# Kernel tuning notes

Hardware: AMD Instinct MI355X
Metric: run time of the kernel (lower is better)

## Reference

```python
import jax, jax.numpy as jnp
import numpy as np

N_NODES = 128
B = 2048
N = B * N_NODES          # 262144 total nodes
E_PER = 512
E = B * E_PER            # 1048576 edges
H = 64                   # hidden_dim == embedding_dim
EPS = 1e-5


def _layernorm(x, g, b):
    m = x.mean(-1, keepdims=True)
    v = ((x - m) ** 2).mean(-1, keepdims=True)
    return (x - m) * jax.lax.rsqrt(v + EPS) * g + b


def setup_inputs() -> dict:
    key = jax.random.key(0)
    ks = jax.random.split(key, 16)
    node_feature = jax.random.randint(ks[0], (N,), 0, N_NODES, dtype=jnp.int32)
    # edges stay within each graph's node block
    offs = (jnp.arange(E, dtype=jnp.int32) // E_PER) * N_NODES
    src = offs + jax.random.randint(ks[1], (E,), 0, N_NODES, dtype=jnp.int32)
    dst = offs + jax.random.randint(ks[2], (E,), 0, N_NODES, dtype=jnp.int32)
    edge_index = jnp.stack([src, dst], axis=1)          # [E, 2]
    batch_ptr = jnp.arange(B + 1, dtype=jnp.int32) * N_NODES
    s = 0.1
    f32 = jnp.float32
    return {
        'node_feature': node_feature,
        'edge_index': edge_index,
        'batch_ptr': batch_ptr,
        'emb': jax.random.normal(ks[3], (N_NODES, H), f32),
        'gcn_w': jax.random.normal(ks[4], (H, H), f32) * s,
        'gcn_b': jnp.zeros((H,), f32),
        'lin1_w': jax.random.normal(ks[5], (H, H), f32) * s,
        'lin1_b': jnp.zeros((H,), f32),
        'lin2_w': jax.random.normal(ks[6], (H, H), f32) * s,
        'lin2_b': jnp.zeros((H,), f32),
        'ln_g': jnp.ones((H,), f32),
        'ln_b': jnp.zeros((H,), f32),
        'ex_w1': jax.random.normal(ks[7], (H, H), f32) * s,
        'ex_b1': jnp.zeros((H,), f32),
        'ex_ln_g': jnp.ones((H,), f32),
        'ex_ln_b': jnp.zeros((H,), f32),
        'ex_w2': jax.random.normal(ks[8], (H, 1), f32) * s,
        'ex_b2': jnp.zeros((1,), f32),
    }


def _forward(node_feature, edge_index, batch_ptr, emb, gcn_w, gcn_b,
             lin1_w, lin1_b, lin2_w, lin2_b, ln_g, ln_b,
             ex_w1, ex_b1, ex_ln_g, ex_ln_b, ex_w2, ex_b2):
    x = emb[node_feature]                                # [N, H] embedding lookup
    # --- GCNConv (PyG gcn_norm: self-loops + symmetric normalization) ---
    loops = jnp.arange(N, dtype=edge_index.dtype)
    src = jnp.concatenate([edge_index[:, 0], loops])
    dst = jnp.concatenate([edge_index[:, 1], loops])
    deg = jax.ops.segment_sum(jnp.ones_like(dst, dtype=x.dtype), dst, N)
    dinv = jnp.where(deg > 0, jax.lax.rsqrt(deg), 0.0)
    norm = dinv[src] * dinv[dst]                         # [E+N]
    h = x @ gcn_w                                        # linear (no bias)
    h = jax.ops.segment_sum(norm[:, None] * h[src], dst, N) + gcn_b
    # --- Linear -> ReLU -> Linear, residual, LayerNorm ---
    h = jnp.maximum(h @ lin1_w + lin1_b, 0.0) @ lin2_w + lin2_b
    ef = _layernorm(h + x, ln_g, ln_b)                   # [N, H]
    # --- cumsum-based group mean over batch_ptr segments ---
    cs = jnp.concatenate([jnp.zeros((1, H), ef.dtype), jnp.cumsum(ef, axis=0)], 0)
    size = (batch_ptr[1:] - batch_ptr[:-1]).astype(ef.dtype)
    means = (cs[batch_ptr[1:]] - cs[batch_ptr[:-1]]) / size[:, None]   # [B, H]
    # --- exit MLP: Linear -> LayerNorm -> ReLU -> Linear ---
    exit_action = jnp.maximum(_layernorm(means @ ex_w1 + ex_b1, ex_ln_g, ex_ln_b), 0.0) @ ex_w2 + ex_b2  # [B, 1]
    # --- pairwise edge logits + triu/tril gather (directed) ---
    efb = ef.reshape(B, N_NODES, H)
    scores = jnp.einsum('bnf,bmf->bnm', efb, efb) / jnp.sqrt(jnp.asarray(H, ef.dtype))
    iu0, iu1 = np.triu_indices(N_NODES, 1)
    il0, il1 = np.tril_indices(N_NODES, -1)
    i0 = jnp.asarray(np.concatenate([iu0, il0]))
    i1 = jnp.asarray(np.concatenate([iu1, il1]))
    edge_actions = scores[:, i0, i1]                     # [B, n^2 - n]
    return jnp.concatenate([edge_actions, exit_action], axis=-1)


def reference(node_feature, edge_index, batch_ptr, emb, gcn_w, gcn_b,
              lin1_w, lin1_b, lin2_w, lin2_b, ln_g, ln_b,
              ex_w1, ex_b1, ex_ln_g, ex_ln_b, ex_w2, ex_b2):
    return _forward(node_feature, edge_index, batch_ptr, emb, gcn_w, gcn_b,
                    lin1_w, lin1_b, lin2_w, lin2_b, ln_g, ln_b,
                    ex_w1, ex_b1, ex_ln_g, ex_ln_b, ex_w2, ex_b2)
```

## Files before the change

### kernel.cpp

```cpp
#include <hip/hip_runtime.h>

typedef __bf16 bf16_t;
typedef __bf16 bf16x8 __attribute__((ext_vector_type(8)));
typedef float  f32x4  __attribute__((ext_vector_type(4)));
typedef f32x4  f32x4u __attribute__((aligned(4)));

#define LDR 72

__device__ __forceinline__ float bflo(unsigned u){ return __uint_as_float(u << 16); }
__device__ __forceinline__ float bfhi(unsigned u){ return __uint_as_float(u & 0xffff0000u); }

#define WS_MAP_OFF 24576

__global__ void prep_kernel(const float* __restrict__ emb,
                            const float* __restrict__ gcn_w,
                            const float* __restrict__ lin1_w,
                            const float* __restrict__ lin2_w,
                            bf16_t* __restrict__ ws)
{
    int t = blockIdx.x * 256 + threadIdx.x;
    bf16_t* emb_bf = ws;
    bf16_t* hw_bf  = ws + 8192;
    bf16_t* w1T    = ws + 16384;
    bf16_t* w2T    = ws + 20480;

    emb_bf[t] = (bf16_t)emb[t];
    int i = t >> 6, j = t & 63;
    float s = 0.f;
    #pragma unroll 8
    for (int k = 0; k < 64; ++k) s += emb[i*64 + k] * gcn_w[k*64 + j];
    hw_bf[t] = (bf16_t)s;
    if (t < 4096){
        int jj = t >> 6, kk = t & 63;
        w1T[t] = (bf16_t)lin1_w[kk*64 + jj];
        w2T[t] = (bf16_t)lin2_w[kk*64 + jj];
    }

    if (blockIdx.x == 0){
        __shared__ bf16_t pA[16*32];
        __shared__ bf16_t pB[16*32];
        int tid = threadIdx.x;
        for (int c = tid; c < 512; c += 256){
            int r = c >> 5, k = c & 31;
            pA[c] = (bf16_t)((k == 0) ? (float)r : ((k == 1) ? 1.f : 0.f));
            pB[c] = (bf16_t)((k == 0) ? 1.f : ((k == 1) ? (float)(128*r) : 0.f));
        }
        __syncthreads();
        if (tid < 64){
            int l15 = tid & 15, lg = tid >> 4;
            bf16x8 a  = *reinterpret_cast<const bf16x8*>(&pA[l15*32 + lg*8]);
            bf16x8 bb = *reinterpret_cast<const bf16x8*>(&pB[l15*32 + lg*8]);
            f32x4 acc = (f32x4){0.f,0.f,0.f,0.f};
            acc = __builtin_amdgcn_mfma_f32_16x16x32_bf16(a, bb, acc, 0, 0, 0);
            int* map = (int*)(ws + WS_MAP_OFF);
            int mi[4], mj[4];
            #pragma unroll
            for (int r = 0; r < 4; ++r){
                int iv = (int)(acc[r] + 0.5f);
                mi[r] = iv & 127; mj[r] = iv >> 7;
                map[tid*4 + r] = mi[r] | (mj[r] << 8);
            }
            bool ok = (mi[0]==mi[1] && mi[1]==mi[2] && mi[2]==mi[3] &&
                       mj[1]==mj[0]+1 && mj[2]==mj[0]+2 && mj[3]==mj[0]+3 &&
                       (mj[0] & 3) == 0);
            unsigned long long all = __ballot(ok);
            if (tid == 0) map[256] = (all == ~0ull) ? 1 : 0;
        }
    }
}

__global__ __launch_bounds__(256, 4) void fused_kernel(
    const int*   __restrict__ node_feature,
    const int*   __restrict__ edge_index,
    const float* __restrict__ gcn_b,
    const float* __restrict__ lin1_b,
    const float* __restrict__ lin2_b,
    const float* __restrict__ ln_g,
    const float* __restrict__ ln_b,
    const float* __restrict__ ex_w1,
    const float* __restrict__ ex_b1,
    const float* __restrict__ ex_ln_g,
    const float* __restrict__ ex_ln_b,
    const float* __restrict__ ex_w2,
    const float* __restrict__ ex_b2,
    const bf16_t* __restrict__ ws,
    float* __restrict__ out)
{
    __shared__ __align__(16) bf16_t bufB[128*LDR];
    __shared__ __align__(16) bf16_t bufC[128*LDR];
    __shared__ __align__(8)  unsigned char pool[2176];
    __shared__ unsigned char s_nf8[128];

    unsigned char* s_adj   = pool;
    int*           s_start = (int*)(pool + 512);
    int*           s_cur   = (int*)(pool + 1040);
    float*         s_dinv  = (float*)(pool + 1552);
    float*         s_pm    = (float*)pool;
    float*         s_means = (float*)(pool + 1024);

    const int tid  = threadIdx.x;
    const int b    = blockIdx.x;
    const int wid  = tid >> 6;
    const int lane = tid & 63;
    const int l15  = lane & 15;
    const int lg   = lane >> 4;
    const long obase = (long)b * 16257;

    const bf16_t* emb_bf = ws;
    const bf16_t* hw_bf  = ws + 8192;
    const bf16_t* w1T    = ws + 16384;
    const bf16_t* w2T    = ws + 20480;

    int mi[4], mj[4], vflag;
    {
        const int* map = (const int*)(ws + WS_MAP_OFF);
        #pragma unroll
        for (int r = 0; r < 4; ++r){
            int m = map[lane*4 + r];
            mi[r] = m & 255; mj[r] = m >> 8;
        }
        vflag = map[256];
    }

    const int2* ei = reinterpret_cast<const int2*>(edge_index) + b*512;
    int2 e0 = ei[tid];
    int2 e1 = ei[tid + 256];

    if (tid < 128) s_nf8[tid] = (unsigned char)node_feature[b*128 + tid];
    else           s_cur[tid - 128] = 0;
    __syncthreads();

    atomicAdd(&s_cur[e0.y & 127], 1);
    atomicAdd(&s_cur[e1.y & 127], 1);
    #pragma unroll
    for (int c = tid; c < 1024; c += 256){
        int row = c >> 3, ch = c & 7;
        uint4 vh = reinterpret_cast<const uint4*>(hw_bf + (int)s_nf8[row]*64)[ch];
        reinterpret_cast<uint4*>(&bufB[row*LDR])[ch] = vh;
    }
    __syncthreads();

    if (tid < 64){
        int a0 = s_cur[2*tid], a1 = s_cur[2*tid+1];
        s_dinv[2*tid]   = rsqrtf((float)(a0 + 1));
        s_dinv[2*tid+1] = rsqrtf((float)(a1 + 1));
        int s = a0 + a1;
        #pragma unroll
        for (int d = 1; d < 64; d <<= 1){
            int v = __shfl_up(s, d);
            if (lane >= d) s += v;
        }
        int excl = s - (a0 + a1);
        s_start[2*tid]   = excl;
        s_start[2*tid+1] = excl + a0;
        if (tid == 63) s_start[128] = 512;
        s_cur[2*tid]   = excl;
        s_cur[2*tid+1] = excl + a0;
    }
    __syncthreads();

    {
        int pos0 = atomicAdd(&s_cur[e0.y & 127], 1);
        s_adj[pos0] = (unsigned char)(e0.x & 127);
        int pos1 = atomicAdd(&s_cur[e1.y & 127], 1);
        s_adj[pos1] = (unsigned char)(e1.x & 127);
    }
    __syncthreads();

    {
        const int n  = tid >> 1;
        const int f0 = (tid & 1) << 5;
        float inner[32];
        #pragma unroll
        for (int f = 0; f < 32; ++f) inner[f] = 0.f;
        const float dn = s_dinv[n];
        {
            const uint4* hv = reinterpret_cast<const uint4*>(&bufB[n*LDR + f0]);
            #pragma unroll
            for (int q = 0; q < 4; ++q){
                uint4 v = hv[q];
                inner[q*8+0] += dn * bflo(v.x); inner[q*8+1] += dn * bfhi(v.x);
                inner[q*8+2] += dn * bflo(v.y); inner[q*8+3] += dn * bfhi(v.y);
                inner[q*8+4] += dn * bflo(v.z); inner[q*8+5] += dn * bfhi(v.z);
                inner[q*8+6] += dn * bflo(v.w); inner[q*8+7] += dn * bfhi(v.w);
            }
        }
        const int st = s_start[n], cn = s_start[n+1] - st;
        for (int k = 0; k < cn; ++k){
            int src = s_adj[st + k];
            float w = s_dinv[src];
            const uint4* hv = reinterpret_cast<const uint4*>(&bufB[src*LDR + f0]);
            #pragma unroll
            for (int q = 0; q < 4; ++q){
                uint4 v = hv[q];
                inner[q*8+0] += w * bflo(v.x); inner[q*8+1] += w * bfhi(v.x);
                inner[q*8+2] += w * bflo(v.y); inner[q*8+3] += w * bfhi(v.y);
                inner[q*8+4] += w * bflo(v.z); inner[q*8+5] += w * bfhi(v.z);
                inner[q*8+6] += w * bflo(v.w); inner[q*8+7] += w * bfhi(v.w);
            }
        }
        const float* gb = gcn_b + f0;
        #pragma unroll
        for (int f = 0; f < 32; ++f)
            bufC[n*LDR + f0 + f] = (bf16_t)(dn * inner[f] + gb[f]);
    }
    __syncthreads();

    {
        bf16x8 af[2][2];
        #pragma unroll
        for (int fm = 0; fm < 2; ++fm)
            #pragma unroll
            for (int kk = 0; kk < 2; ++kk)
                af[fm][kk] = *reinterpret_cast<const bf16x8*>(
                    &bufC[(wid*32 + fm*16 + l15)*LDR + kk*32 + lg*8]);
        f32x4 acc[2][4];
        #pragma unroll
        for (int fm = 0; fm < 2; ++fm)
            #pragma unroll
            for (int fn = 0; fn < 4; ++fn)
                acc[fm][fn] = (f32x4){0.f,0.f,0.f,0.f};
        #pragma unroll
        for (int fn = 0; fn < 4; ++fn)
            #pragma unroll
            for (int kk = 0; kk < 2; ++kk){
                bf16x8 bfr = *reinterpret_cast<const bf16x8*>(
                    &w1T[(fn*16 + l15)*64 + kk*32 + lg*8]);
                #pragma unroll
                for (int fm = 0; fm < 2; ++fm)
                    acc[fm][fn] = __builtin_amdgcn_mfma_f32_16x16x32_bf16(
                        af[fm][kk], bfr, acc[fm][fn], 0, 0, 0);
            }
        #pragma unroll
        for (int fm = 0; fm < 2; ++fm)
            #pragma unroll
            for (int fn = 0; fn < 4; ++fn)
                #pragma unroll
                for (int r = 0; r < 4; ++r){
                    int row = wid*32 + fm*16 + mi[r];
                    int col = fn*16 + mj[r];
                    bufB[row*LDR + col] = (bf16_t)fmaxf(acc[fm][fn][r] + lin1_b[col], 0.f);
                }
    }
    __syncthreads();

    {
        bf16x8 af[2][2];
        #pragma unroll
        for (int fm = 0; fm < 2; ++fm)
            #pragma unroll
            for (int kk = 0; kk < 2; ++kk)
                af[fm][kk] = *reinterpret_cast<const bf16x8*>(
                    &bufB[(wid*32 + fm*16 + l15)*LDR + kk*32 + lg*8]);
        f32x4 acc[2][4];
        #pragma unroll
        for (int fm = 0; fm < 2; ++fm)
            #pragma unroll
            for (int fn = 0; fn < 4; ++fn)
                acc[fm][fn] = (f32x4){0.f,0.f,0.f,0.f};
        #pragma unroll
        for (int fn = 0; fn < 4; ++fn)
            #pragma unroll
            for (int kk = 0; kk < 2; ++kk){
                bf16x8 bfr = *reinterpret_cast<const bf16x8*>(
                    &w2T[(fn*16 + l15)*64 + kk*32 + lg*8]);
                #pragma unroll
                for (int fm = 0; fm < 2; ++fm)
                    acc[fm][fn] = __builtin_amdgcn_mfma_f32_16x16x32_bf16(
                        af[fm][kk], bfr, acc[fm][fn], 0, 0, 0);
            }
        #pragma unroll
        for (int fm = 0; fm < 2; ++fm)
            #pragma unroll
            for (int fn = 0; fn < 4; ++fn)
                #pragma unroll
                for (int r = 0; r < 4; ++r){
                    int row = wid*32 + fm*16 + mi[r];
                    int col = fn*16 + mj[r];
                    bufC[row*LDR + col] = (bf16_t)(acc[fm][fn][r] + lin2_b[col]);
                }
    }
    __syncthreads();

    {
        const int n  = tid >> 1;
        const int f0 = (tid & 1) << 5;
        const bf16x8* xp = reinterpret_cast<const bf16x8*>(&emb_bf[(int)s_nf8[n]*64 + f0]);
        const bf16x8* rp = reinterpret_cast<const bf16x8*>(&bufC[n*LDR + f0]);
        float vv[32];
        float p1 = 0.f, p2 = 0.f;
        #pragma unroll
        for (int q = 0; q < 4; ++q){
            bf16x8 v8 = rp[q];
            bf16x8 x8 = xp[q];
            #pragma unroll
            for (int e = 0; e < 8; ++e){
                float f = (float)v8[e] + (float)x8[e];
                vv[q*8+e] = f; p1 += f; p2 += f*f;
            }
        }
        p1 += __shfl_xor(p1, 1);
        p2 += __shfl_xor(p2, 1);
        float mean = p1 * 0.015625f;
        float var  = p2 * 0.015625f - mean*mean;
        float rstd = rsqrtf(var + 1e-5f);
        const float* lg_ = ln_g + f0;
        const float* lb_ = ln_b + f0;
        #pragma unroll
        for (int j = 0; j < 32; ++j)
            bufC[n*LDR + f0 + j] = (bf16_t)((vv[j] - mean) * rstd * lg_[j] + lb_[j]);
    }
    __syncthreads();

    {
        int col = tid & 63, q = tid >> 6;
        float s = 0.f;
        #pragma unroll 8
        for (int r = q*32; r < q*32 + 32; ++r)
            s += (float)bufC[r*LDR + col];
        s_pm[q*64 + col] = s;
    }
    __syncthreads();
    if (tid < 64)
        s_means[tid] = (s_pm[tid] + s_pm[64+tid] + s_pm[128+tid] + s_pm[192+tid]) * 0.0078125f;
    __syncthreads();

    if (tid < 64){
        float a = ex_b1[lane];
        #pragma unroll 8
        for (int k = 0; k < 64; ++k)
            a += s_means[k] * ex_w1[k*64 + lane];
        float p1 = a, p2 = a*a;
        #pragma unroll
        for (int m = 1; m < 64; m <<= 1){ p1 += __shfl_xor(p1, m); p2 += __shfl_xor(p2, m); }
        float mean = p1 * 0.015625f;
        float var  = p2 * 0.015625f - mean*mean;
        float u = (a - mean) * rsqrtf(var + 1e-5f) * ex_ln_g[lane] + ex_ln_b[lane];
        u = fmaxf(u, 0.f);
        float prod = u * ex_w2[lane];
        #pragma unroll
        for (int m = 1; m < 64; m <<= 1) prod += __shfl_xor(prod, m);
        if (lane == 0) out[obase + 16256] = prod + ex_b2[0];
    }

    {
        bf16x8 af[2][2];
        #pragma unroll
        for (int fm = 0; fm < 2; ++fm)
            #pragma unroll
            for (int kk = 0; kk < 2; ++kk)
                af[fm][kk] = *reinterpret_cast<const bf16x8*>(
                    &bufC[(wid*32 + fm*16 + l15)*LDR + kk*32 + lg*8]);
        f32x4 acc[2][8];
        #pragma unroll
        for (int fm = 0; fm < 2; ++fm)
            #pragma unroll
            for (int fn = 0; fn < 8; ++fn)
                acc[fm][fn] = (f32x4){0.f,0.f,0.f,0.f};
        #pragma unroll
        for (int fn = 0; fn < 8; ++fn)
            #pragma unroll
            for (int kk = 0; kk < 2; ++kk){
                bf16x8 bfr = *reinterpret_cast<const bf16x8*>(
                    &bufC[(fn*16 + l15)*LDR + kk*32 + lg*8]);
                #pragma unroll
                for (int fm = 0; fm < 2; ++fm)
                    acc[fm][fn] = __builtin_amdgcn_mfma_f32_16x16x32_bf16(
                        af[fm][kk], bfr, acc[fm][fn], 0, 0, 0);
            }
        float* ob = out + obase;
        if (vflag){
            #pragma unroll
            for (int fm = 0; fm < 2; ++fm){
                int i = wid*32 + fm*16 + mi[0];
                int tri = (i*(i-1)) >> 1;
                int c_tu = i*127 - tri - i - 1;
                int c_tl = 8128 + tri;
                #pragma unroll
                for (int fn = 0; fn < 8; ++fn){
                    int jb = fn*16 + mj[0];
                    f32x4 w = acc[fm][fn] * 0.125f;
                    if (i < jb){
                        *reinterpret_cast<f32x4u*>(ob + c_tu + jb) = w;
                    } else if (i > jb + 3){
                        *reinterpret_cast<f32x4u*>(ob + c_tl + jb) = w;
                    } else {
                        #pragma unroll
                        for (int r = 0; r < 4; ++r){
                            int j = jb + r;
                            if (i != j)
                                ob[(i < j) ? (c_tu + j) : (c_tl + j)] = w[r];
                        }
                    }
                }
            }
        } else {
            #pragma unroll
            for (int fm = 0; fm < 2; ++fm){
                #pragma unroll
                for (int fn = 0; fn < 8; ++fn){
                    #pragma unroll
                    for (int r = 0; r < 4; ++r){
                        int i = wid*32 + fm*16 + mi[r];
                        int j = fn*16 + mj[r];
                        if (i != j){
                            float v = acc[fm][fn][r] * 0.125f;
                            int p = (i < j) ? (i*127 - ((i*(i-1)) >> 1) + j - i - 1)
                                            : (8128 + ((i*(i-1)) >> 1) + j);
                            ob[p] = v;
                        }
                    }
                }
            }
        }
    }
}

extern "C" void kernel_launch(void* const* d_in, const int* in_sizes, int n_in,
                              void* d_out, int out_size, void* d_ws, size_t ws_size,
                              hipStream_t stream)
{
    const int*   node_feature = (const int*)  d_in[0];
    const int*   edge_index   = (const int*)  d_in[1];
    const float* emb     = (const float*)d_in[3];
    const float* gcn_w   = (const float*)d_in[4];
    const float* gcn_b   = (const float*)d_in[5];
    const float* lin1_w  = (const float*)d_in[6];
    const float* lin1_b  = (const float*)d_in[7];
    const float* lin2_w  = (const float*)d_in[8];
    const float* lin2_b  = (const float*)d_in[9];
    const float* ln_g    = (const float*)d_in[10];
    const float* ln_b    = (const float*)d_in[11];
    const float* ex_w1   = (const float*)d_in[12];
    const float* ex_b1   = (const float*)d_in[13];
    const float* ex_ln_g = (const float*)d_in[14];
    const float* ex_ln_b = (const float*)d_in[15];
    const float* ex_w2   = (const float*)d_in[16];
    const float* ex_b2   = (const float*)d_in[17];
    bf16_t* ws  = (bf16_t*)d_ws;
    float*  out = (float*)d_out;

    prep_kernel<<<32, 256, 0, stream>>>(emb, gcn_w, lin1_w, lin2_w, ws);
    fused_kernel<<<2048, 256, 0, stream>>>(node_feature, edge_index,
        gcn_b, lin1_b, lin2_b, ln_g, ln_b,
        ex_w1, ex_b1, ex_ln_g, ex_ln_b, ex_w2, ex_b2,
        ws, out);
}
```

Baseline: 71.86 us.

## Add transposed-fragment vector store path, stage biases in LDS, use wave-local fences

```diff
diff --git a/kernel.cpp b/kernel.cpp
--- a/kernel.cpp
+++ b/kernel.cpp
@@ -9,6 +9,10 @@
 
 __device__ __forceinline__ float bflo(unsigned u){ return __uint_as_float(u << 16); }
 __device__ __forceinline__ float bfhi(unsigned u){ return __uint_as_float(u & 0xffff0000u); }
+__device__ __forceinline__ void lds_fence(){
+    asm volatile("s_waitcnt lgkmcnt(0)" ::: "memory");
+    __builtin_amdgcn_sched_barrier(0);
+}
 
 #define WS_MAP_OFF 24576
 
@@ -60,11 +64,18 @@
                 mi[r] = iv & 127; mj[r] = iv >> 7;
                 map[tid*4 + r] = mi[r] | (mj[r] << 8);
             }
-            bool ok = (mi[0]==mi[1] && mi[1]==mi[2] && mi[2]==mi[3] &&
+            bool c1 = (mi[0]==mi[1] && mi[1]==mi[2] && mi[2]==mi[3] &&
                        mj[1]==mj[0]+1 && mj[2]==mj[0]+2 && mj[3]==mj[0]+3 &&
                        (mj[0] & 3) == 0);
-            unsigned long long all = __ballot(ok);
-            if (tid == 0) map[256] = (all == ~0ull) ? 1 : 0;
+            bool c2 = (mj[0]==mj[1] && mj[1]==mj[2] && mj[2]==mj[3] &&
+                       mi[1]==mi[0]+1 && mi[2]==mi[0]+2 && mi[3]==mi[0]+3 &&
+                       (mi[0] & 3) == 0);
+            unsigned long long b1 = __ballot(c1);
+            unsigned long long b2 = __ballot(c2);
+            if (tid == 0){
+                map[256] = (b1 == ~0ull) ? 1 : 0;
+                map[257] = (b2 == ~0ull) ? 1 : 0;
+            }
         }
     }
 }
@@ -90,6 +101,7 @@
     __shared__ __align__(16) bf16_t bufC[128*LDR];
     __shared__ __align__(8)  unsigned char pool[2176];
     __shared__ unsigned char s_nf8[128];
+    __shared__ float s_b[320];
 
     unsigned char* s_adj   = pool;
     int*           s_start = (int*)(pool + 512);
@@ -111,7 +123,7 @@
     const bf16_t* w1T    = ws + 16384;
     const bf16_t* w2T    = ws + 20480;
 
-    int mi[4], mj[4], vflag;
+    int mi[4], mj[4], flag1, flag2;
     {
         const int* map = (const int*)(ws + WS_MAP_OFF);
         #pragma unroll
@@ -119,7 +131,8 @@
             int m = map[lane*4 + r];
             mi[r] = m & 255; mj[r] = m >> 8;
         }
-        vflag = map[256];
+        flag1 = map[256];
+        flag2 = map[257];
     }
 
     const int2* ei = reinterpret_cast<const int2*>(edge_index) + b*512;
@@ -127,7 +140,17 @@
     int2 e1 = ei[tid + 256];
 
     if (tid < 128) s_nf8[tid] = (unsigned char)node_feature[b*128 + tid];
-    else           s_cur[tid - 128] = 0;
+    else if (tid < 192){
+        int j = tid - 128;
+        s_b[j]       = gcn_b[j];
+        s_b[64 + j]  = lin1_b[j];
+        s_b[128 + j] = lin2_b[j];
+        s_b[192 + j] = ln_g[j];
+        s_b[256 + j] = ln_b[j];
+        s_cur[j] = 0;
+    } else {
+        s_cur[tid - 192 + 64] = 0;
+    }
     __syncthreads();
 
     atomicAdd(&s_cur[e0.y & 127], 1);
@@ -167,6 +190,7 @@
     }
     __syncthreads();
 
+
     {
         const int n  = tid >> 1;
         const int f0 = (tid & 1) << 5;
@@ -199,12 +223,11 @@
                 inner[q*8+6] += w * bflo(v.w); inner[q*8+7] += w * bfhi(v.w);
             }
         }
-        const float* gb = gcn_b + f0;
         #pragma unroll
         for (int f = 0; f < 32; ++f)
-            bufC[n*LDR + f0 + f] = (bf16_t)(dn * inner[f] + gb[f]);
-    }
-    __syncthreads();
+            bufC[n*LDR + f0 + f] = (bf16_t)(dn * inner[f] + s_b[f0 + f]);
+    }
+    lds_fence();
 
     {
         bf16x8 af[2][2];
@@ -239,10 +262,10 @@
                 for (int r = 0; r < 4; ++r){
                     int row = wid*32 + fm*16 + mi[r];
                     int col = fn*16 + mj[r];
-                    bufB[row*LDR + col] = (bf16_t)fmaxf(acc[fm][fn][r] + lin1_b[col], 0.f);
+                    bufC[row*LDR + col] = (bf16_t)fmaxf(acc[fm][fn][r] + s_b[64 + col], 0.f);
                 }
     }
-    __syncthreads();
+    lds_fence();
 
     {
         bf16x8 af[2][2];
@@ -251,7 +274,7 @@
             #pragma unroll
             for (int kk = 0; kk < 2; ++kk)
                 af[fm][kk] = *reinterpret_cast<const bf16x8*>(
-                    &bufB[(wid*32 + fm*16 + l15)*LDR + kk*32 + lg*8]);
+                    &bufC[(wid*32 + fm*16 + l15)*LDR + kk*32 + lg*8]);
         f32x4 acc[2][4];
         #pragma unroll
         for (int fm = 0; fm < 2; ++fm)
@@ -277,10 +300,10 @@
                 for (int r = 0; r < 4; ++r){
                     int row = wid*32 + fm*16 + mi[r];
                     int col = fn*16 + mj[r];
-                    bufC[row*LDR + col] = (bf16_t)(acc[fm][fn][r] + lin2_b[col]);
+                    bufC[row*LDR + col] = (bf16_t)(acc[fm][fn][r] + s_b[128 + col]);
                 }
     }
-    __syncthreads();
+    lds_fence();
 
     {
         const int n  = tid >> 1;
@@ -304,11 +327,9 @@
         float mean = p1 * 0.015625f;
         float var  = p2 * 0.015625f - mean*mean;
         float rstd = rsqrtf(var + 1e-5f);
-        const float* lg_ = ln_g + f0;
-        const float* lb_ = ln_b + f0;
         #pragma unroll
         for (int j = 0; j < 32; ++j)
-            bufC[n*LDR + f0 + j] = (bf16_t)((vv[j] - mean) * rstd * lg_[j] + lb_[j]);
+            bufC[n*LDR + f0 + j] = (bf16_t)((vv[j] - mean) * rstd * s_b[192 + f0 + j] + s_b[256 + f0 + j]);
     }
     __syncthreads();
 
@@ -369,7 +390,31 @@
                         af[fm][kk], bfr, acc[fm][fn], 0, 0, 0);
             }
         float* ob = out + obase;
-        if (vflag){
+        if (flag2){
+            #pragma unroll
+            for (int fm = 0; fm < 2; ++fm){
+                int I = wid*32 + fm*16 + mi[0];
+                #pragma unroll
+                for (int fn = 0; fn < 8; ++fn){
+                    int J = fn*16 + mj[0];
+                    int tri = (J*(J-1)) >> 1;
+                    f32x4 w = acc[fm][fn] * 0.125f;
+                    if (J < I){
+                        *reinterpret_cast<f32x4u*>(ob + J*127 - tri - J - 1 + I) = w;
+                    } else if (J > I + 3){
+                        *reinterpret_cast<f32x4u*>(ob + 8128 + tri + I) = w;
+                    } else {
+                        #pragma unroll
+                        for (int r = 0; r < 4; ++r){
+                            int c = I + r;
+                            if (c != J)
+                                ob[(J < c) ? (J*127 - tri - J - 1 + c)
+                                           : (8128 + tri + c)] = w[r];
+                        }
+                    }
+                }
+            }
+        } else if (flag1){
             #pragma unroll
             for (int fm = 0; fm < 2; ++fm){
                 int i = wid*32 + fm*16 + mi[0];
```

New measurement: 73.24 us. About the same (+1.9%).

## Fuse GCN aggregation into lin1 MFMA, stage biases in LDS, drop vector stores

Applied to the files above, without the earlier changes.

```diff
diff --git a/kernel.cpp b/kernel.cpp
--- a/kernel.cpp
+++ b/kernel.cpp
@@ -3,12 +3,15 @@
 typedef __bf16 bf16_t;
 typedef __bf16 bf16x8 __attribute__((ext_vector_type(8)));
 typedef float  f32x4  __attribute__((ext_vector_type(4)));
-typedef f32x4  f32x4u __attribute__((aligned(4)));
 
 #define LDR 72
 
 __device__ __forceinline__ float bflo(unsigned u){ return __uint_as_float(u << 16); }
 __device__ __forceinline__ float bfhi(unsigned u){ return __uint_as_float(u & 0xffff0000u); }
+__device__ __forceinline__ void lds_fence(){
+    asm volatile("s_waitcnt lgkmcnt(0)" ::: "memory");
+    __builtin_amdgcn_sched_barrier(0);
+}
 
 #define WS_MAP_OFF 24576
 
@@ -53,18 +56,11 @@
             f32x4 acc = (f32x4){0.f,0.f,0.f,0.f};
             acc = __builtin_amdgcn_mfma_f32_16x16x32_bf16(a, bb, acc, 0, 0, 0);
             int* map = (int*)(ws + WS_MAP_OFF);
-            int mi[4], mj[4];
             #pragma unroll
             for (int r = 0; r < 4; ++r){
                 int iv = (int)(acc[r] + 0.5f);
-                mi[r] = iv & 127; mj[r] = iv >> 7;
-                map[tid*4 + r] = mi[r] | (mj[r] << 8);
-            }
-            bool ok = (mi[0]==mi[1] && mi[1]==mi[2] && mi[2]==mi[3] &&
-                       mj[1]==mj[0]+1 && mj[2]==mj[0]+2 && mj[3]==mj[0]+3 &&
-                       (mj[0] & 3) == 0);
-            unsigned long long all = __ballot(ok);
-            if (tid == 0) map[256] = (all == ~0ull) ? 1 : 0;
+                map[tid*4 + r] = (iv & 127) | ((iv >> 7) << 8);
+            }
         }
     }
 }
@@ -90,6 +86,7 @@
     __shared__ __align__(16) bf16_t bufC[128*LDR];
     __shared__ __align__(8)  unsigned char pool[2176];
     __shared__ unsigned char s_nf8[128];
+    __shared__ float s_b[320];
 
     unsigned char* s_adj   = pool;
     int*           s_start = (int*)(pool + 512);
@@ -111,7 +108,7 @@
     const bf16_t* w1T    = ws + 16384;
     const bf16_t* w2T    = ws + 20480;
 
-    int mi[4], mj[4], vflag;
+    int mi[4], mj[4];
     {
         const int* map = (const int*)(ws + WS_MAP_OFF);
         #pragma unroll
@@ -119,7 +116,6 @@
             int m = map[lane*4 + r];
             mi[r] = m & 255; mj[r] = m >> 8;
         }
-        vflag = map[256];
     }
 
     const int2* ei = reinterpret_cast<const int2*>(edge_index) + b*512;
@@ -127,7 +123,17 @@
     int2 e1 = ei[tid + 256];
 
     if (tid < 128) s_nf8[tid] = (unsigned char)node_feature[b*128 + tid];
-    else           s_cur[tid - 128] = 0;
+    else if (tid < 192){
+        int j = tid - 128;
+        s_b[j]       = gcn_b[j];
+        s_b[64 + j]  = lin1_b[j];
+        s_b[128 + j] = lin2_b[j];
+        s_b[192 + j] = ln_g[j];
+        s_b[256 + j] = ln_b[j];
+        s_cur[j] = 0;
+    } else {
+        s_cur[tid - 192 + 64] = 0;
+    }
     __syncthreads();
 
     atomicAdd(&s_cur[e0.y & 127], 1);
@@ -168,43 +174,87 @@
     __syncthreads();
 
     {
-        const int n  = tid >> 1;
-        const int f0 = (tid & 1) << 5;
-        float inner[32];
-        #pragma unroll
-        for (int f = 0; f < 32; ++f) inner[f] = 0.f;
-        const float dn = s_dinv[n];
-        {
-            const uint4* hv = reinterpret_cast<const uint4*>(&bufB[n*LDR + f0]);
-            #pragma unroll
-            for (int q = 0; q < 4; ++q){
-                uint4 v = hv[q];
-                inner[q*8+0] += dn * bflo(v.x); inner[q*8+1] += dn * bfhi(v.x);
-                inner[q*8+2] += dn * bflo(v.y); inner[q*8+3] += dn * bfhi(v.y);
-                inner[q*8+4] += dn * bflo(v.z); inner[q*8+5] += dn * bfhi(v.z);
-                inner[q*8+6] += dn * bflo(v.w); inner[q*8+7] += dn * bfhi(v.w);
-            }
-        }
-        const int st = s_start[n], cn = s_start[n+1] - st;
-        for (int k = 0; k < cn; ++k){
-            int src = s_adj[st + k];
-            float w = s_dinv[src];
-            const uint4* hv = reinterpret_cast<const uint4*>(&bufB[src*LDR + f0]);
-            #pragma unroll
-            for (int q = 0; q < 4; ++q){
-                uint4 v = hv[q];
-                inner[q*8+0] += w * bflo(v.x); inner[q*8+1] += w * bfhi(v.x);
-                inner[q*8+2] += w * bflo(v.y); inner[q*8+3] += w * bfhi(v.y);
-                inner[q*8+4] += w * bflo(v.z); inner[q*8+5] += w * bfhi(v.z);
-                inner[q*8+6] += w * bflo(v.w); inner[q*8+7] += w * bfhi(v.w);
-            }
-        }
-        const float* gb = gcn_b + f0;
-        #pragma unroll
-        for (int f = 0; f < 32; ++f)
-            bufC[n*LDR + f0 + f] = (bf16_t)(dn * inner[f] + gb[f]);
-    }
-    __syncthreads();
+        float inner[2][16];
+        float dnv[2];
+        #pragma unroll
+        for (int fm = 0; fm < 2; ++fm)
+            #pragma unroll
+            for (int f = 0; f < 16; ++f) inner[fm][f] = 0.f;
+
+        #pragma unroll
+        for (int fm = 0; fm < 2; ++fm){
+            const int row = wid*32 + fm*16 + l15;
+            const float dn = s_dinv[row];
+            dnv[fm] = dn;
+            {
+                uint4 c0 = *reinterpret_cast<const uint4*>(&bufB[row*LDR + lg*8]);
+                uint4 c1 = *reinterpret_cast<const uint4*>(&bufB[row*LDR + 32 + lg*8]);
+                inner[fm][0]  += dn * bflo(c0.x); inner[fm][1]  += dn * bfhi(c0.x);
+                inner[fm][2]  += dn * bflo(c0.y); inner[fm][3]  += dn * bfhi(c0.y);
+                inner[fm][4]  += dn * bflo(c0.z); inner[fm][5]  += dn * bfhi(c0.z);
+                inner[fm][6]  += dn * bflo(c0.w); inner[fm][7]  += dn * bfhi(c0.w);
+                inner[fm][8]  += dn * bflo(c1.x); inner[fm][9]  += dn * bfhi(c1.x);
+                inner[fm][10] += dn * bflo(c1.y); inner[fm][11] += dn * bfhi(c1.y);
+                inner[fm][12] += dn * bflo(c1.z); inner[fm][13] += dn * bfhi(c1.z);
+                inner[fm][14] += dn * bflo(c1.w); inner[fm][15] += dn * bfhi(c1.w);
+            }
+            const int st = s_start[row], cn = s_start[row+1] - st;
+            for (int k = 0; k < cn; ++k){
+                int src = s_adj[st + k];
+                float w = s_dinv[src];
+                uint4 c0 = *reinterpret_cast<const uint4*>(&bufB[src*LDR + lg*8]);
+                uint4 c1 = *reinterpret_cast<const uint4*>(&bufB[src*LDR + 32 + lg*8]);
+                inner[fm][0]  += w * bflo(c0.x); inner[fm][1]  += w * bfhi(c0.x);
+                inner[fm][2]  += w * bflo(c0.y); inner[fm][3]  += w * bfhi(c0.y);
+                inner[fm][4]  += w * bflo(c0.z); inner[fm][5]  += w * bfhi(c0.z);
+                inner[fm][6]  += w * bflo(c0.w); inner[fm][7]  += w * bfhi(c0.w);
+                inner[fm][8]  += w * bflo(c1.x); inner[fm][9]  += w * bfhi(c1.x);
+                inner[fm][10] += w * bflo(c1.y); inner[fm][11] += w * bfhi(c1.y);
+                inner[fm][12] += w * bflo(c1.z); inner[fm][13] += w * bfhi(c1.z);
+                inner[fm][14] += w * bflo(c1.w); inner[fm][15] += w * bfhi(c1.w);
+            }
+        }
+
+        bf16x8 af[2][2];
+        #pragma unroll
+        for (int fm = 0; fm < 2; ++fm)
+            #pragma unroll
+            for (int kk = 0; kk < 2; ++kk)
+                #pragma unroll
+                for (int e = 0; e < 8; ++e){
+                    int col = kk*32 + lg*8 + e;
+                    af[fm][kk][e] = (bf16_t)(dnv[fm]*inner[fm][kk*8 + e] + s_b[col]);
+                }
+
+        f32x4 acc[2][4];
+        #pragma unroll
+        for (int fm = 0; fm < 2; ++fm)
+            #pragma unroll
+            for (int fn = 0; fn < 4; ++fn)
+                acc[fm][fn] = (f32x4){0.f,0.f,0.f,0.f};
+        #pragma unroll
+        for (int fn = 0; fn < 4; ++fn)
+            #pragma unroll
+            for (int kk = 0; kk < 2; ++kk){
+                bf16x8 bfr = *reinterpret_cast<const bf16x8*>(
+                    &w1T[(fn*16 + l15)*64 + kk*32 + lg*8]);
+                #pragma unroll
+                for (int fm = 0; fm < 2; ++fm)
+                    acc[fm][fn] = __builtin_amdgcn_mfma_f32_16x16x32_bf16(
+                        af[fm][kk], bfr, acc[fm][fn], 0, 0, 0);
+            }
+        #pragma unroll
+        for (int fm = 0; fm < 2; ++fm)
+            #pragma unroll
+            for (int fn = 0; fn < 4; ++fn)
+                #pragma unroll
+                for (int r = 0; r < 4; ++r){
+                    int row = wid*32 + fm*16 + mi[r];
+                    int col = fn*16 + mj[r];
+                    bufC[row*LDR + col] = (bf16_t)fmaxf(acc[fm][fn][r] + s_b[64 + col], 0.f);
+                }
+    }
+    lds_fence();
 
     {
         bf16x8 af[2][2];
@@ -225,7 +275,7 @@
             #pragma unroll
             for (int kk = 0; kk < 2; ++kk){
                 bf16x8 bfr = *reinterpret_cast<const bf16x8*>(
-                    &w1T[(fn*16 + l15)*64 + kk*32 + lg*8]);
+                    &w2T[(fn*16 + l15)*64 + kk*32 + lg*8]);
                 #pragma unroll
                 for (int fm = 0; fm < 2; ++fm)
                     acc[fm][fn] = __builtin_amdgcn_mfma_f32_16x16x32_bf16(
@@ -239,48 +289,10 @@
                 for (int r = 0; r < 4; ++r){
                     int row = wid*32 + fm*16 + mi[r];
                     int col = fn*16 + mj[r];
-                    bufB[row*LDR + col] = (bf16_t)fmaxf(acc[fm][fn][r] + lin1_b[col], 0.f);
+                    bufC[row*LDR + col] = (bf16_t)(acc[fm][fn][r] + s_b[128 + col]);
                 }
     }
-    __syncthreads();
-
-    {
-        bf16x8 af[2][2];
-        #pragma unroll
-        for (int fm = 0; fm < 2; ++fm)
-            #pragma unroll
-            for (int kk = 0; kk < 2; ++kk)
-                af[fm][kk] = *reinterpret_cast<const bf16x8*>(
-                    &bufB[(wid*32 + fm*16 + l15)*LDR + kk*32 + lg*8]);
-        f32x4 acc[2][4];
-        #pragma unroll
-        for (int fm = 0; fm < 2; ++fm)
-            #pragma unroll
-            for (int fn = 0; fn < 4; ++fn)
-                acc[fm][fn] = (f32x4){0.f,0.f,0.f,0.f};
-        #pragma unroll
-        for (int fn = 0; fn < 4; ++fn)
-            #pragma unroll
-            for (int kk = 0; kk < 2; ++kk){
-                bf16x8 bfr = *reinterpret_cast<const bf16x8*>(
-                    &w2T[(fn*16 + l15)*64 + kk*32 + lg*8]);
-                #pragma unroll
-                for (int fm = 0; fm < 2; ++fm)
-                    acc[fm][fn] = __builtin_amdgcn_mfma_f32_16x16x32_bf16(
-                        af[fm][kk], bfr, acc[fm][fn], 0, 0, 0);
-            }
-        #pragma unroll
-        for (int fm = 0; fm < 2; ++fm)
-            #pragma unroll
-            for (int fn = 0; fn < 4; ++fn)
-                #pragma unroll
-                for (int r = 0; r < 4; ++r){
-                    int row = wid*32 + fm*16 + mi[r];
-                    int col = fn*16 + mj[r];
-                    bufC[row*LDR + col] = (bf16_t)(acc[fm][fn][r] + lin2_b[col]);
-                }
-    }
-    __syncthreads();
+    lds_fence();
 
     {
         const int n  = tid >> 1;
@@ -304,11 +316,9 @@
         float mean = p1 * 0.015625f;
         float var  = p2 * 0.015625f - mean*mean;
         float rstd = rsqrtf(var + 1e-5f);
-        const float* lg_ = ln_g + f0;
-        const float* lb_ = ln_b + f0;
         #pragma unroll
         for (int j = 0; j < 32; ++j)
-            bufC[n*LDR + f0 + j] = (bf16_t)((vv[j] - mean) * rstd * lg_[j] + lb_[j]);
+            bufC[n*LDR + f0 + j] = (bf16_t)((vv[j] - mean) * rstd * s_b[192 + f0 + j] + s_b[256 + f0 + j]);
     }
     __syncthreads();
 
@@ -369,46 +379,19 @@
                         af[fm][kk], bfr, acc[fm][fn], 0, 0, 0);
             }
         float* ob = out + obase;
-        if (vflag){
-            #pragma unroll
-            for (int fm = 0; fm < 2; ++fm){
-                int i = wid*32 + fm*16 + mi[0];
-                int tri = (i*(i-1)) >> 1;
-                int c_tu = i*127 - tri - i - 1;
-                int c_tl = 8128 + tri;
-                #pragma unroll
-                for (int fn = 0; fn < 8; ++fn){
-                    int jb = fn*16 + mj[0];
-                    f32x4 w = acc[fm][fn] * 0.125f;
-                    if (i < jb){
-                        *reinterpret_cast<f32x4u*>(ob + c_tu + jb) = w;
-                    } else if (i > jb + 3){
-                        *reinterpret_cast<f32x4u*>(ob + c_tl + jb) = w;
-                    } else {
-                        #pragma unroll
-                        for (int r = 0; r < 4; ++r){
-                            int j = jb + r;
-                            if (i != j)
-                                ob[(i < j) ? (c_tu + j) : (c_tl + j)] = w[r];
-                        }
-                    }
-                }
-            }
-        } else {
-            #pragma unroll
-            for (int fm = 0; fm < 2; ++fm){
-                #pragma unroll
-                for (int fn = 0; fn < 8; ++fn){
-                    #pragma unroll
-                    for (int r = 0; r < 4; ++r){
-                        int i = wid*32 + fm*16 + mi[r];
-                        int j = fn*16 + mj[r];
-                        if (i != j){
-                            float v = acc[fm][fn][r] * 0.125f;
-                            int p = (i < j) ? (i*127 - ((i*(i-1)) >> 1) + j - i - 1)
-                                            : (8128 + ((i*(i-1)) >> 1) + j);
-                            ob[p] = v;
-                        }
+        #pragma unroll
+        for (int fm = 0; fm < 2; ++fm){
+            #pragma unroll
+            for (int fn = 0; fn < 8; ++fn){
+                #pragma unroll
+                for (int r = 0; r < 4; ++r){
+                    int i = wid*32 + fm*16 + mi[r];
+                    int j = fn*16 + mj[r];
+                    if (i != j){
+                        float v = acc[fm][fn][r] * 0.125f;
+                        int p = (i < j) ? (i*127 - ((i*(i-1)) >> 1) + j - i - 1)
+                                        : (8128 + ((i*(i-1)) >> 1) + j);
+                        ob[p] = v;
                     }
                 }
             }
```

Result: faster. 61.71 us (-14.1%).
